# Kernel optimization log

Measured on AMD Instinct MI355X. Metric: run time of the kernel, lower is better.

The kernel has to match this reference:

```python
import jax, jax.numpy as jnp
import numpy as np
from jax.scipy.special import logsumexp

B, S, L = 1024, 8192, 3


def setup_inputs() -> dict:
    key = jax.random.key(0)
    k1, k2, k3, k4, k5 = jax.random.split(key, 5)
    emissions = jax.random.normal(k1, (B, S, L), dtype=jnp.float32)
    labels = jax.random.randint(k2, (B, S), 0, L, dtype=jnp.int64)
    start_transitions = 0.1 * jax.random.normal(k3, (L,), dtype=jnp.float32)
    transitions = 0.1 * jax.random.normal(k4, (L, L), dtype=jnp.float32)
    end_transitions = 0.1 * jax.random.normal(k5, (L,), dtype=jnp.float32)
    return {
        "emissions": emissions,
        "labels": labels,
        "start_transitions": start_transitions,
        "transitions": transitions,
        "end_transitions": end_transitions,
    }


def reference(emissions, labels, start_transitions, transitions, end_transitions):
    # mask is all-ones in the original module, so every timestep is valid.
    # --- log partition via forward algorithm (sequential DP over time) ---
    alpha0 = start_transitions[None, :] + emissions[:, 0]  # [B, L]

    def step(alpha, e_t):
        # alpha: [B, L] (prev label), e_t: [B, L] (next label)
        nxt = logsumexp(alpha[:, :, None] + transitions[None, :, :] + e_t[:, None, :], axis=1)
        return nxt, None

    e_rest = jnp.swapaxes(emissions[:, 1:], 0, 1)  # [S-1, B, L]
    alphaT, _ = jax.lax.scan(step, alpha0, e_rest)
    log_z = logsumexp(alphaT + end_transitions[None, :], axis=-1)  # [B]

    # --- gold path score ---
    em_score = jnp.take_along_axis(emissions, labels[:, :, None], axis=2)[..., 0].sum(axis=1)  # [B]
    trans_score = transitions[labels[:, :-1], labels[:, 1:]].sum(axis=1)  # [B]
    score = start_transitions[labels[:, 0]] + em_score + trans_score + end_transitions[labels[:, -1]]

    log_likelihood = jnp.sum(score - log_z)  # torchcrf default reduction='sum'
    return -log_likelihood
```

## Files before the change

### kernel.cpp

```cpp
#include <hip/hip_runtime.h>

#define LOG2E 1.44269504088896340736f
#define LN2   0.69314718055994530942f
#define S_    8192
#define HALF  4096
#define TPB   512
#define KPT   8
#define NWAVE 8

#if __has_builtin(__builtin_amdgcn_exp2f)
__device__ __forceinline__ float exp2f_(float x){ return __builtin_amdgcn_exp2f(x); }
#else
__device__ __forceinline__ float exp2f_(float x){ return __expf(x * LN2); }
#endif
#if __has_builtin(__builtin_amdgcn_logf)
__device__ __forceinline__ float log2f_(float x){ return __builtin_amdgcn_logf(x); }
#else
__device__ __forceinline__ float log2f_(float x){ return __logf(x) * LOG2E; }
#endif

__device__ __forceinline__ void renorm9(float* V, float& s){
    float m = fmaxf(fmaxf(fmaxf(V[0],V[1]),fmaxf(V[2],V[3])),
                    fmaxf(fmaxf(V[4],V[5]),fmaxf(V[6],V[7])));
    m = fmaxf(m, V[8]);
    int e = (__float_as_int(m) >> 23) & 0xff;
    float rs = __int_as_float((254 - e) << 23);
#pragma unroll
    for (int k=0;k<9;++k) V[k] *= rs;
    s += (float)(e - 127);
}

__device__ __forceinline__ void mul33(float* C, const float* A, const float* B){
#pragma unroll
    for (int i=0;i<3;i++){
        float a0=A[i*3], a1=A[i*3+1], a2=A[i*3+2];
#pragma unroll
        for (int j=0;j<3;j++)
            C[i*3+j] = a0*B[j] + a1*B[3+j] + a2*B[6+j];
    }
}

extern "C" __global__ __launch_bounds__(TPB, 4)
void crf_fwd(const float* __restrict__ em, const int* __restrict__ lab,
             const float* __restrict__ stt, const float* __restrict__ trt,
             const float* __restrict__ ent, float* __restrict__ ws)
{
    const int bid = blockIdx.x;
    const int b = bid >> 1, h = bid & 1;
    const int tid = threadIdx.x;
    const int ln = tid & 63, wv = tid >> 6;

    __shared__ float4 emS[6*513];
    __shared__ int4   labS[2*513];
    __shared__ float  wM[NWAVE][10];
    __shared__ float  wSc[NWAVE];
    __shared__ float  tT[9], tS[3];

    const float4* emG = (const float4*)(em + ((size_t)b*S_ + (size_t)h*HALF)*3);
    const int4*   lbG = (const int4*)(lab + ((size_t)b*S_ + (size_t)h*HALF));

    float4 er0=emG[tid],      er1=emG[512+tid],  er2=emG[1024+tid],
           er3=emG[1536+tid], er4=emG[2048+tid], er5=emG[2560+tid];
    int4   lr0=lbG[tid],      lr1=lbG[512+tid];
    int prevg = 0;
    if (tid==0 && h==1) prevg = ((const int*)lbG)[-1];

    if (tid < 9) tT[tid] = trt[tid];
    if (tid < 3) tS[tid] = stt[tid];

    float W00=__expf(trt[0]), W01=__expf(trt[1]), W02=__expf(trt[2]);
    float W10=__expf(trt[3]), W11=__expf(trt[4]), W12=__expf(trt[5]);
    float W20=__expf(trt[6]), W21=__expf(trt[7]), W22=__expf(trt[8]);

    {
        #define EMW(k, reg) { int sg=(k)*512+tid; int T=sg/6; int j=sg-T*6; emS[j*513+T]=reg; }
        EMW(0,er0) EMW(1,er1) EMW(2,er2) EMW(3,er3) EMW(4,er4) EMW(5,er5)
        #undef EMW
        { int sg = tid;       labS[(sg&1)*513 + (sg>>1)] = lr0; }
        { int sg = 512 + tid; labS[(sg&1)*513 + (sg>>1)] = lr1; }
    }
    __syncthreads();

    const int t = tid;
    float ew[24];
    *(float4*)&ew[0]  = emS[t];        *(float4*)&ew[4]  = emS[513+t];
    *(float4*)&ew[8]  = emS[2*513+t];  *(float4*)&ew[12] = emS[3*513+t];
    *(float4*)&ew[16] = emS[4*513+t];  *(float4*)&ew[20] = emS[5*513+t];
    int lw[8];
    *(int4*)&lw[0] = labS[t];  *(int4*)&lw[4] = labS[513+t];

    int prev;
    if (t > 0) prev = ((const int*)labS)[(513 + (t-1))*4 + 3];
    else       prev = prevg;

    float V[9] = {1,0,0, 0,1,0, 0,0,1};
    float S2 = 0.f, sc = 0.f;
    const bool head = (h==0 && t==0);
#pragma unroll
    for (int s=0; s<KPT; ++s){
        float ea=ew[3*s], eb=ew[3*s+1], ec=ew[3*s+2];
        int l = lw[s];
        float ee = (l==1) ? eb : ((l==2) ? ec : ea);
        if (s==0 && head) sc += tS[l] + ee;
        else              sc += tT[prev*3+l] + ee;
        prev = l;
        if (!(s==0 && head)) {
            float E0=__expf(ea), E1=__expf(eb), E2=__expf(ec);
#pragma unroll
            for (int i=0;i<3;i++){
                float a0=V[i*3], a1=V[i*3+1], a2=V[i*3+2];
                V[i*3]  =(a0*W00+a1*W10+a2*W20)*E0;
                V[i*3+1]=(a0*W01+a1*W11+a2*W21)*E1;
                V[i*3+2]=(a0*W02+a1*W12+a2*W22)*E2;
            }
        }
        if (s==3 || s==7) renorm9(V, S2);
    }

#pragma unroll
    for (int off=1; off<64; off<<=1){
        float bv[9];
#pragma unroll
        for (int k=0;k<9;++k) bv[k] = __shfl_down(V[k], (unsigned)off, 64);
        float bs2 = __shfl_down(S2, (unsigned)off, 64);
        float C[9]; mul33(C, V, bv);
        S2 += bs2;
        renorm9(C, S2);
#pragma unroll
        for (int k=0;k<9;++k) V[k]=C[k];
    }
#pragma unroll
    for (int off=32; off; off>>=1) sc += __shfl_down(sc, (unsigned)off, 64);

    if (ln==0){
#pragma unroll
        for (int k=0;k<9;++k) wM[wv][k]=V[k];
        wM[wv][9]=S2; wSc[wv]=sc;
    }
    __syncthreads();

    if (tid==0){
        float A[9], As = wM[0][9], scT = wSc[0];
#pragma unroll
        for (int k=0;k<9;++k) A[k]=wM[0][k];
#pragma unroll
        for (int w=1; w<NWAVE; ++w){
            float C[9]; mul33(C, A, wM[w]);
            As += wM[w][9];
            renorm9(C, As);
#pragma unroll
            for (int k=0;k<9;++k) A[k]=C[k];
            scT += wSc[w];
        }
        float* r = ws + (size_t)bid*16;
#pragma unroll
        for (int k=0;k<9;++k) r[k]=A[k];
        r[9]=As; r[10]=scT;
        float4 e0 = emS[0];
        r[11]=e0.x; r[12]=e0.y; r[13]=e0.z;
    }
}

extern "C" __global__ __launch_bounds__(1024)
void crf_fin(const float* __restrict__ ws, const float* __restrict__ stt,
             const float* __restrict__ ent, float* __restrict__ out, int B)
{
    const int b = threadIdx.x;
    float nll = 0.f;
    if (b < B){
        const float* r0 = ws + (size_t)(2*b)*16;
        const float* r1 = ws + (size_t)(2*b+1)*16;
        float C[9];
#pragma unroll
        for (int i=0;i<3;i++){
            float a0=r0[i*3], a1=r0[i*3+1], a2=r0[i*3+2];
#pragma unroll
            for (int j=0;j<3;j++)
                C[i*3+j] = a0*r1[j] + a1*r1[3+j] + a2*r1[6+j];
        }
        float S  = r0[9] + r1[9];
        float sc = r0[10] + r1[10];
        float a0=(stt[0]+r0[11])*LOG2E, a1=(stt[1]+r0[12])*LOG2E, a2=(stt[2]+r0[13])*LOG2E;
        float am = fmaxf(fmaxf(a0,a1),a2);
        float w0=exp2f_(a0-am), w1=exp2f_(a1-am), w2=exp2f_(a2-am);
        float q0=w0*C[0]+w1*C[3]+w2*C[6];
        float q1=w0*C[1]+w1*C[4]+w2*C[7];
        float q2=w0*C[2]+w1*C[5]+w2*C[8];
        float z = q0*exp2f_(ent[0]*LOG2E) + q1*exp2f_(ent[1]*LOG2E) + q2*exp2f_(ent[2]*LOG2E);
        float logz = (am + S + log2f_(z)) * LN2;
        nll = logz - sc;
    }
#pragma unroll
    for (int off=32; off; off>>=1) nll += __shfl_down(nll, (unsigned)off, 64);
    __shared__ float acc[16];
    if ((threadIdx.x & 63)==0) acc[threadIdx.x>>6] = nll;
    __syncthreads();
    if (threadIdx.x==0){
        float s=0.f;
#pragma unroll
        for (int k=0;k<16;++k) s += acc[k];
        out[0] = s;
    }
}

extern "C" void kernel_launch(void* const* d_in, const int* in_sizes, int n_in,
                              void* d_out, int out_size, void* d_ws, size_t ws_size,
                              hipStream_t stream) {
    const float* em  = (const float*)d_in[0];
    const int*   lab = (const int*)d_in[1];
    const float* stt = (const float*)d_in[2];
    const float* trt = (const float*)d_in[3];
    const float* ent = (const float*)d_in[4];
    float* out = (float*)d_out;
    float* ws  = (float*)d_ws;

    const int B = in_sizes[1] / S_;
    crf_fwd<<<2*B, TPB, 0, stream>>>(em, lab, stt, trt, ent, ws);
    crf_fin<<<1, 1024, 0, stream>>>(ws, stt, ent, out, B);
}
```

Before: 187.4 us.

## Split sequences into four chunks and stage emissions with direct global-to-LDS loads

Each batch row is now split into four 2048-step chunks handled by 256-thread blocks instead of two 4096-step halves on 512-thread blocks. Emissions are copied straight into LDS with the global_load_lds builtin in contiguous layout, which replaces the register round-trip and transposed padded layout. Labels are read directly from global memory, and the previous label comes from a wave shuffle. The finalize kernel now chains four partial transfer matrices per row instead of two, without renormalising between them. That adds risk of overflow and also bank conflicts on the stride-6 float4 LDS reads.

```diff
diff --git a/kernel.cpp b/kernel.cpp
--- a/kernel.cpp
+++ b/kernel.cpp
@@ -3,10 +3,11 @@
 #define LOG2E 1.44269504088896340736f
 #define LN2   0.69314718055994530942f
 #define S_    8192
-#define HALF  4096
-#define TPB   512
+#define CHUNK 2048
+#define NCH   4
+#define TPB   256
 #define KPT   8
-#define NWAVE 8
+#define NWAVE 4
 
 #if __has_builtin(__builtin_amdgcn_exp2f)
 __device__ __forceinline__ float exp2f_(float x){ return __builtin_amdgcn_exp2f(x); }
@@ -19,6 +20,15 @@
 __device__ __forceinline__ float log2f_(float x){ return __logf(x) * LOG2E; }
 #endif
 
+__device__ __forceinline__ void gload16(const void* g, void* l, int ln){
+#if __has_builtin(__builtin_amdgcn_global_load_lds)
+    __builtin_amdgcn_global_load_lds((const __attribute__((address_space(1))) void*)g,
+                                     (__attribute__((address_space(3))) void*)l, 16, 0, 0);
+#else
+    *(float4*)((char*)l + ln*16) = *(const float4*)g;
+#endif
+}
+
 __device__ __forceinline__ void renorm9(float* V, float& s){
     float m = fmaxf(fmaxf(fmaxf(V[0],V[1]),fmaxf(V[2],V[3])),
                     fmaxf(fmaxf(V[4],V[5]),fmaxf(V[6],V[7])));
@@ -40,71 +50,68 @@
     }
 }
 
-extern "C" __global__ __launch_bounds__(TPB, 4)
+extern "C" __global__ __launch_bounds__(TPB)
 void crf_fwd(const float* __restrict__ em, const int* __restrict__ lab,
              const float* __restrict__ stt, const float* __restrict__ trt,
              const float* __restrict__ ent, float* __restrict__ ws)
 {
     const int bid = blockIdx.x;
-    const int b = bid >> 1, h = bid & 1;
-    const int tid = threadIdx.x;
-    const int ln = tid & 63, wv = tid >> 6;
-
-    __shared__ float4 emS[6*513];
-    __shared__ int4   labS[2*513];
+    const int b = bid >> 2, h = bid & 3;
+    const int tid = threadIdx.x, ln = tid & 63, wv = tid >> 6;
+
+    __shared__ float4 emS[CHUNK*3/4];
+    __shared__ float  tT[9];
     __shared__ float  wM[NWAVE][10];
     __shared__ float  wSc[NWAVE];
-    __shared__ float  tT[9], tS[3];
-
-    const float4* emG = (const float4*)(em + ((size_t)b*S_ + (size_t)h*HALF)*3);
-    const int4*   lbG = (const int4*)(lab + ((size_t)b*S_ + (size_t)h*HALF));
-
-    float4 er0=emG[tid],      er1=emG[512+tid],  er2=emG[1024+tid],
-           er3=emG[1536+tid], er4=emG[2048+tid], er5=emG[2560+tid];
-    int4   lr0=lbG[tid],      lr1=lbG[512+tid];
-    int prevg = 0;
-    if (tid==0 && h==1) prevg = ((const int*)lbG)[-1];
-
+
+    const float* emB = em + ((size_t)b*S_ + (size_t)h*CHUNK)*3;
+    const int*   lbB = lab + (size_t)b*S_ + h*CHUNK;
+
+    {
+        const char* gb = (const char*)emB;
+        char* lb = (char*)&emS[0];
+#pragma unroll
+        for (int k=0;k<6;++k){
+            int c = k*NWAVE + wv;
+            gload16(gb + c*1024 + ln*16, lb + c*1024, ln);
+        }
+    }
     if (tid < 9) tT[tid] = trt[tid];
-    if (tid < 3) tS[tid] = stt[tid];
+
+    const int4* lb4 = (const int4*)lbB;
+    int4 lv0 = lb4[2*tid], lv1 = lb4[2*tid+1];
 
     float W00=__expf(trt[0]), W01=__expf(trt[1]), W02=__expf(trt[2]);
     float W10=__expf(trt[3]), W11=__expf(trt[4]), W12=__expf(trt[5]);
     float W20=__expf(trt[6]), W21=__expf(trt[7]), W22=__expf(trt[8]);
 
+    const bool head = (h==0 && tid==0);
+    int prev_sh = __shfl_up(lv1.w, 1, 64);
+    int prev;
+    if (ln == 0) prev = head ? 0 : lbB[tid*KPT - 1];
+    else         prev = prev_sh;
+
+    __syncthreads();
+
+    float ew[24];
     {
-        #define EMW(k, reg) { int sg=(k)*512+tid; int T=sg/6; int j=sg-T*6; emS[j*513+T]=reg; }
-        EMW(0,er0) EMW(1,er1) EMW(2,er2) EMW(3,er3) EMW(4,er4) EMW(5,er5)
-        #undef EMW
-        { int sg = tid;       labS[(sg&1)*513 + (sg>>1)] = lr0; }
-        { int sg = 512 + tid; labS[(sg&1)*513 + (sg>>1)] = lr1; }
-    }
-    __syncthreads();
-
-    const int t = tid;
-    float ew[24];
-    *(float4*)&ew[0]  = emS[t];        *(float4*)&ew[4]  = emS[513+t];
-    *(float4*)&ew[8]  = emS[2*513+t];  *(float4*)&ew[12] = emS[3*513+t];
-    *(float4*)&ew[16] = emS[4*513+t];  *(float4*)&ew[20] = emS[5*513+t];
-    int lw[8];
-    *(int4*)&lw[0] = labS[t];  *(int4*)&lw[4] = labS[513+t];
-
-    int prev;
-    if (t > 0) prev = ((const int*)labS)[(513 + (t-1))*4 + 3];
-    else       prev = prevg;
+        const float4* p = &emS[tid*6];
+        *(float4*)&ew[0]  = p[0]; *(float4*)&ew[4]  = p[1]; *(float4*)&ew[8]  = p[2];
+        *(float4*)&ew[12] = p[3]; *(float4*)&ew[16] = p[4]; *(float4*)&ew[20] = p[5];
+    }
+    int lw[8] = {lv0.x,lv0.y,lv0.z,lv0.w, lv1.x,lv1.y,lv1.z,lv1.w};
 
     float V[9] = {1,0,0, 0,1,0, 0,0,1};
     float S2 = 0.f, sc = 0.f;
-    const bool head = (h==0 && t==0);
 #pragma unroll
     for (int s=0; s<KPT; ++s){
         float ea=ew[3*s], eb=ew[3*s+1], ec=ew[3*s+2];
         int l = lw[s];
         float ee = (l==1) ? eb : ((l==2) ? ec : ea);
-        if (s==0 && head) sc += tS[l] + ee;
+        if (head && s==0) sc += stt[l] + ee;
         else              sc += tT[prev*3+l] + ee;
         prev = l;
-        if (!(s==0 && head)) {
+        if (!(head && s==0)) {
             float E0=__expf(ea), E1=__expf(eb), E2=__expf(ec);
 #pragma unroll
             for (int i=0;i<3;i++){
@@ -156,8 +163,7 @@
 #pragma unroll
         for (int k=0;k<9;++k) r[k]=A[k];
         r[9]=As; r[10]=scT;
-        float4 e0 = emS[0];
-        r[11]=e0.x; r[12]=e0.y; r[13]=e0.z;
+        r[11]=ew[0]; r[12]=ew[1]; r[13]=ew[2];
     }
 }
 
@@ -168,19 +174,19 @@
     const int b = threadIdx.x;
     float nll = 0.f;
     if (b < B){
-        const float* r0 = ws + (size_t)(2*b)*16;
-        const float* r1 = ws + (size_t)(2*b+1)*16;
-        float C[9];
-#pragma unroll
-        for (int i=0;i<3;i++){
-            float a0=r0[i*3], a1=r0[i*3+1], a2=r0[i*3+2];
-#pragma unroll
-            for (int j=0;j<3;j++)
-                C[i*3+j] = a0*r1[j] + a1*r1[3+j] + a2*r1[6+j];
-        }
-        float S  = r0[9] + r1[9];
-        float sc = r0[10] + r1[10];
-        float a0=(stt[0]+r0[11])*LOG2E, a1=(stt[1]+r0[12])*LOG2E, a2=(stt[2]+r0[13])*LOG2E;
+        const float* rr = ws + (size_t)b*NCH*16;
+        float C[9], S = rr[9], sc = rr[10];
+#pragma unroll
+        for (int k=0;k<9;++k) C[k]=rr[k];
+#pragma unroll
+        for (int q=1;q<NCH;++q){
+            const float* r = rr + q*16;
+            float T[9]; mul33(T, C, r);
+#pragma unroll
+            for (int k=0;k<9;++k) C[k]=T[k];
+            S += r[9]; sc += r[10];
+        }
+        float a0=(stt[0]+rr[11])*LOG2E, a1=(stt[1]+rr[12])*LOG2E, a2=(stt[2]+rr[13])*LOG2E;
         float am = fmaxf(fmaxf(a0,a1),a2);
         float w0=exp2f_(a0-am), w1=exp2f_(a1-am), w2=exp2f_(a2-am);
         float q0=w0*C[0]+w1*C[3]+w2*C[6];
@@ -215,6 +221,6 @@
     float* ws  = (float*)d_ws;
 
     const int B = in_sizes[1] / S_;
-    crf_fwd<<<2*B, TPB, 0, stream>>>(em, lab, stt, trt, ent, ws);
+    crf_fwd<<<NCH*B, TPB, 0, stream>>>(em, lab, stt, trt, ent, ws);
     crf_fin<<<1, 1024, 0, stream>>>(ws, stt, ent, out, B);
 }
```

Result: slower. 191.4 us (+2.1%).
